# Optimization experiments

Hardware: AMD Instinct MI355X
Metric: run time of the kernel (lower is better)

The kernel has to match this reference:

```python
import jax, jax.numpy as jnp
import numpy as np

TOP_K = 2  # num_expert in the torch module


def setup_inputs() -> dict:
    key = jax.random.key(0)
    ks = jax.random.split(key, 8)
    B, C, H, W, E, Dh = 8, 512, 32, 32, 8, 1024
    inputs = jax.random.normal(ks[0], (B, C, H, W), dtype=jnp.float32)
    k = jax.random.uniform(ks[1], (B, 1, 1, 1), dtype=jnp.float32)
    # gate: global-avg-pool + Linear(C -> E)
    Wg = jax.random.normal(ks[2], (C, E), dtype=jnp.float32) / np.sqrt(C)
    bg = jnp.zeros((E,), dtype=jnp.float32)
    # experts: per-expert 2-layer channel MLP (1x1-conv style), modulated by k
    W1 = jax.random.normal(ks[3], (E, C, Dh), dtype=jnp.float32) / np.sqrt(C)
    b1 = jnp.zeros((E, Dh), dtype=jnp.float32)
    W2 = jax.random.normal(ks[4], (E, Dh, C), dtype=jnp.float32) / np.sqrt(Dh)
    b2 = jnp.zeros((E, C), dtype=jnp.float32)
    return {"inputs": inputs, "k": k, "Wg": Wg, "bg": bg,
            "W1": W1, "b1": b1, "W2": W2, "b2": b2}


def reference(inputs, k, Wg, bg, W1, b1, W2, b2):
    B = inputs.shape[0]
    # --- gate: softmax in fp32, cast back (matches F.softmax(dtype=torch.float)) ---
    logits = jnp.mean(inputs, axis=(2, 3)) @ Wg + bg            # [B, E]
    weights = jax.nn.softmax(logits.astype(jnp.float32), axis=1).astype(inputs.dtype)
    topk_w, topk_idx = jax.lax.top_k(weights, TOP_K)            # [B, K]
    # --- scatter top-k gate weights into dense [B, E] mask (training path) ---
    exp_w = jnp.zeros_like(weights).at[jnp.arange(B)[:, None], topk_idx].set(topk_w)
    # --- run ALL experts densely (training-mode math), masked combine ---
    h = jnp.einsum('bchw,ecd->bedhw', inputs, W1) + b1[None, :, :, None, None]
    h = jax.nn.gelu(h, approximate=False)                        # [B,E,Dh,H,W]
    y = jnp.einsum('bedhw,edc->bechw', h, W2) + b2[None, :, :, None, None]
    y = y * k[:, None]                                           # per-sample scalar mod
    out = inputs + jnp.einsum('bechw,be->bchw', y, exp_w)        # residual + weighted sum
    return out
```

## Files before the change

### kernel.cpp

```cpp
#include <hip/hip_runtime.h>
#include <hip/hip_bf16.h>
#include <math.h>


typedef __bf16 bf16_t;
typedef __attribute__((ext_vector_type(8))) __bf16 bf16x8;
typedef __attribute__((ext_vector_type(4))) __bf16 bf16x4;
typedef __attribute__((ext_vector_type(4))) float f32x4;

#define GLDS(g, l) __builtin_amdgcn_global_load_lds(                      \
    (const __attribute__((address_space(1))) void*)(const void*)(g),       \
    (__attribute__((address_space(3))) void*)(void*)(l), 16, 0, 0)

__device__ __forceinline__ int xcd_swz(int bid, int grid) {
    return (bid & 7) * (grid >> 3) + (bid >> 3);
}

__device__ __forceinline__ float gelu_fast(float x) {
    float z = x * 0.70710678118654752f;
    float az = fabsf(z);
    float t = 1.0f / (1.0f + 0.3275911f * az);
    float p = ((((1.061405429f * t - 1.453152027f) * t + 1.421413741f) * t
                - 0.284496736f) * t + 0.254829592f) * t;
    float e = __expf(-az * az);
    float er = copysignf(1.0f - p * e, z);
    return 0.5f * x * (1.0f + er);
}

__global__ __launch_bounds__(256) void transpose_cvt_all(
    const float* __restrict__ x, const float* __restrict__ W1,
    const float* __restrict__ W2, bf16_t* __restrict__ xT,
    bf16_t* __restrict__ W1t, bf16_t* __restrict__ W2t, float* __restrict__ pp) {
    int id = blockIdx.x;
    const float* src; bf16_t* dst; int Rows, Cols, csh; bool dm = false;
    if (id < 1024)      { src = x;  dst = xT;  Rows = 512;  Cols = 1024; csh = 4; dm = true; }
    else if (id < 2048) { id -= 1024; src = W1; dst = W1t; Rows = 512;  Cols = 1024; csh = 4; }
    else                { id -= 2048; src = W2; dst = W2t; Rows = 1024; Cols = 512; csh = 3; }
    const int bz = id >> 7, t = id & 127;
    const int ct = t & ((1 << csh) - 1), rt = t >> csh;
    const int r0 = rt * 64, c0 = ct * 64;
    __shared__ float tile[64][65];
    const int tid = threadIdx.x;
    const int lrw = tid >> 4, lcol = (tid & 15) * 4;
    const float* sb = src + (size_t)bz * Rows * Cols + c0;
    #pragma unroll
    for (int p = 0; p < 4; ++p) {
        const int row = p * 16 + lrw;
        float4 v = *(const float4*)(sb + (size_t)(r0 + row) * Cols + lcol);
        tile[row][lcol + 0] = v.x; tile[row][lcol + 1] = v.y;
        tile[row][lcol + 2] = v.z; tile[row][lcol + 3] = v.w;
    }
    __syncthreads();
    if (dm) {
        const int row = tid >> 2, q = tid & 3;
        float s = 0.f;
        #pragma unroll
        for (int j = 0; j < 16; ++j) s += tile[row][q * 16 + j];
        s += __shfl_down(s, 2, 4);
        s += __shfl_down(s, 1, 4);
        if (q == 0) pp[(bz * 16 + ct) * 512 + r0 + row] = s;
    }
    bf16_t* db = dst + (size_t)bz * Rows * Cols + r0;
    #pragma unroll
    for (int q = 0; q < 2; ++q) {
        const int idq = q * 256 + tid;
        const int orow = idq >> 3, seg = idq & 7;
        bf16_t ov[8];
        #pragma unroll
        for (int j = 0; j < 8; ++j) ov[j] = (bf16_t)tile[seg * 8 + j][orow];
        *(bf16x8*)(db + (size_t)(c0 + orow) * Rows + seg * 8) = *(bf16x8*)ov;
    }
}

__global__ void gate_kernel(const float* __restrict__ pp, const float* __restrict__ Wg,
                            const float* __restrict__ bg, const float* __restrict__ kmod,
                            int* __restrict__ tidx, float* __restrict__ scale) {
    const int b = blockIdx.x;
    const int tid = threadIdx.x;
    const int lane = tid & 63, wave = tid >> 6;
    float a[8] = {0.f, 0.f, 0.f, 0.f, 0.f, 0.f, 0.f, 0.f};
    #pragma unroll
    for (int rep = 0; rep < 2; ++rep) {
        const int c = rep * 256 + tid;
        float m = 0.f;
        #pragma unroll
        for (int ht = 0; ht < 16; ++ht) m += pp[(b * 16 + ht) * 512 + c];
        #pragma unroll
        for (int e = 0; e < 8; ++e) a[e] += m * Wg[c * 8 + e];
    }
    #pragma unroll
    for (int e = 0; e < 8; ++e)
        #pragma unroll
        for (int off = 32; off; off >>= 1) a[e] += __shfl_xor(a[e], off, 64);
    __shared__ float red[4][8];
    if (lane == 0) {
        #pragma unroll
        for (int e = 0; e < 8; ++e) red[wave][e] = a[e];
    }
    __syncthreads();
    if (tid == 0) {
        float lg[8], mx = -1e30f;
        #pragma unroll
        for (int e = 0; e < 8; ++e) {
            lg[e] = (red[0][e] + red[1][e] + red[2][e] + red[3][e]) * (1.0f / 1024.0f) + bg[e];
            mx = fmaxf(mx, lg[e]);
        }
        float sum = 0.f;
        #pragma unroll
        for (int e = 0; e < 8; ++e) { lg[e] = expf(lg[e] - mx); sum += lg[e]; }
        float inv = 1.0f / sum;
        float best = -1.f; int i0 = 0;
        for (int j = 0; j < 8; ++j) { float w = lg[j] * inv; if (w > best) { best = w; i0 = j; } }
        float best2 = -1.f; int i1 = 0;
        for (int j = 0; j < 8; ++j) { if (j == i0) continue; float w = lg[j] * inv; if (w > best2) { best2 = w; i1 = j; } }
        float kb = kmod[b];
        tidx[b * 2] = i0; tidx[b * 2 + 1] = i1;
        scale[b * 2] = best * kb; scale[b * 2 + 1] = best2 * kb;
    }
}

__global__ __launch_bounds__(256, 4) void gemm1_kernel(
    const bf16_t* __restrict__ W1t, const bf16_t* __restrict__ xT,
    const float* __restrict__ b1, const int* __restrict__ tidx,
    const float* __restrict__ scale, bf16_t* __restrict__ hT) {
    __shared__ bf16_t smem[17408];
    const int bid = xcd_swz(blockIdx.x, 1024);
    const int pair = bid >> 6, rem = bid & 63;
    const int b = pair >> 1, slot = pair & 1;
    const int e = tidx[pair];
    const float s = scale[pair];
    const int d0 = (rem >> 3) * 128, n0 = (rem & 7) * 128;
    const int tid = threadIdx.x;
    const int lane = tid & 63, wave = tid >> 6;
    const int wm = (wave & 1) * 64, wn = (wave >> 1) * 64;
    const int lrow = lane & 15, quad = lane >> 4;

    const bf16_t* gA = W1t + (size_t)e * 524288 + (size_t)d0 * 512;
    const bf16_t* gB = xT + (size_t)b * 524288 + (size_t)n0 * 512;

    f32x4 acc[4][4];
    #pragma unroll
    for (int i = 0; i < 4; ++i)
        #pragma unroll
        for (int j = 0; j < 4; ++j) acc[i][j] = (f32x4){0.f, 0.f, 0.f, 0.f};

    for (int it = 0; it < 8; ++it) {
        const int k0 = it * 64;
        #pragma unroll
        for (int p = 0; p < 4; ++p) {
            const int row = p * 32 + (tid >> 3);
            const int cg = ((tid & 7) ^ (row & 7)) * 8;
            GLDS(gA + (size_t)row * 512 + k0 + cg, smem + (p * 256 + tid) * 8);
            GLDS(gB + (size_t)row * 512 + k0 + cg, smem + 8192 + (p * 256 + tid) * 8);
        }
        __syncthreads();
        #pragma unroll
        for (int kh = 0; kh < 2; ++kh) {
            const int swz = ((kh * 4 + quad) ^ (lrow & 7)) * 8;
            bf16x8 af[4], bfr[4];
            #pragma unroll
            for (int i = 0; i < 4; ++i) {
                af[i]  = *(const bf16x8*)&smem[(wm + i * 16 + lrow) * 64 + swz];
                bfr[i] = *(const bf16x8*)&smem[8192 + (wn + i * 16 + lrow) * 64 + swz];
            }
            #pragma unroll
            for (int i = 0; i < 4; ++i)
                #pragma unroll
                for (int j = 0; j < 4; ++j)
                    acc[i][j] = __builtin_amdgcn_mfma_f32_16x16x32_bf16(af[i], bfr[j], acc[i][j], 0, 0, 0);
        }
        __syncthreads();
    }

    bf16_t* hTb = hT + (size_t)b * 2097152 + slot * 1024;
    #pragma unroll
    for (int i = 0; i < 4; ++i) {
        const int d_l = wm + i * 16 + quad * 4;
        const float4 bb = *(const float4*)(b1 + e * 1024 + d0 + d_l);
        #pragma unroll
        for (int j = 0; j < 4; ++j) {
            const int hw_l = wn + j * 16 + lrow;
            f32x4 a = acc[i][j];
            bf16x4 o = { (bf16_t)(gelu_fast(a[0] + bb.x) * s),
                         (bf16_t)(gelu_fast(a[1] + bb.y) * s),
                         (bf16_t)(gelu_fast(a[2] + bb.z) * s),
                         (bf16_t)(gelu_fast(a[3] + bb.w) * s) };
            *(bf16x4*)&smem[hw_l * 136 + d_l] = o;
        }
    }
    __syncthreads();
    #pragma unroll
    for (int q = 0; q < 8; ++q) {
        const int idx = q * 256 + tid;
        const int row = idx >> 4, c16 = idx & 15;
        bf16x8 v = *(const bf16x8*)&smem[row * 136 + c16 * 8];
        *(bf16x8*)(hTb + (size_t)(n0 + row) * 2048 + d0 + c16 * 8) = v;
    }
}

__global__ __launch_bounds__(256, 2) void gemm2_kernel(
    const bf16_t* __restrict__ W2t, const bf16_t* __restrict__ hT,
    const float* __restrict__ b2, const int* __restrict__ tidx,
    const float* __restrict__ scale, const float* __restrict__ x,
    float* __restrict__ out) {
    __shared__ bf16_t smem[24576];
    const int bid = xcd_swz(blockIdx.x, 512);
    const int b = bid >> 6, rem = bid & 63;
    const int c0 = (rem >> 3) * 64, hw0 = (rem & 7) * 128;
    const int e0 = tidx[b * 2], e1 = tidx[b * 2 + 1];
    const float s0 = scale[b * 2], s1 = scale[b * 2 + 1];
    const int tid = threadIdx.x;
    const int lane = tid & 63, wave = tid >> 6;
    const int wm = (wave & 1) * 64;
    const int wc = (wave >> 1) * 32;
    const int lrow = lane & 15, quad = lane >> 4;

    const bf16_t* hTb = hT + (size_t)b * 2097152 + (size_t)hw0 * 2048;
    const bf16_t* B0 = W2t + (size_t)e0 * 524288 + (size_t)c0 * 1024;
    const bf16_t* B1 = W2t + (size_t)e1 * 524288 + (size_t)c0 * 1024;

    f32x4 acc[4][2];
    #pragma unroll
    for (int i = 0; i < 4; ++i)
        #pragma unroll
        for (int j = 0; j < 2; ++j) acc[i][j] = (f32x4){0.f, 0.f, 0.f, 0.f};

    auto stage = [&](int st, int it) {
        const int k0 = it * 64;
        bf16_t* dst = smem + st * 12288;
        #pragma unroll
        for (int p = 0; p < 4; ++p) {
            const int row = p * 32 + (tid >> 3);
            const int cg = ((tid & 7) ^ (row & 7)) * 8;
            GLDS(hTb + (size_t)row * 2048 + k0 + cg, dst + (p * 256 + tid) * 8);
        }
        const bf16_t* gB = ((it < 16) ? B0 : B1) + (k0 & 1023);
        #pragma unroll
        for (int p = 0; p < 2; ++p) {
            const int row = p * 32 + (tid >> 3);
            const int cg = ((tid & 7) ^ (row & 7)) * 8;
            GLDS(gB + (size_t)row * 1024 + cg, dst + 8192 + (p * 256 + tid) * 8);
        }
    };

    stage(0, 0);
    __syncthreads();

    for (int it = 0; it < 32; ++it) {
        const int cur = it & 1;
        if (it < 31) stage(cur ^ 1, it + 1);
        const bf16_t* cA = smem + cur * 12288;
        const bf16_t* cB = cA + 8192;
        #pragma unroll
        for (int kh = 0; kh < 2; ++kh) {
            const int swz = ((kh * 4 + quad) ^ (lrow & 7)) * 8;
            bf16x8 af[4], bfr[2];
            #pragma unroll
            for (int i = 0; i < 4; ++i)
                af[i] = *(const bf16x8*)&cA[(wm + i * 16 + lrow) * 64 + swz];
            #pragma unroll
            for (int j = 0; j < 2; ++j)
                bfr[j] = *(const bf16x8*)&cB[(wc + j * 16 + lrow) * 64 + swz];
            #pragma unroll
            for (int i = 0; i < 4; ++i)
                #pragma unroll
                for (int j = 0; j < 2; ++j)
                    acc[i][j] = __builtin_amdgcn_mfma_f32_16x16x32_bf16(af[i], bfr[j], acc[i][j], 0, 0, 0);
        }
        __syncthreads();
    }

    #pragma unroll
    for (int j = 0; j < 2; ++j) {
        const int c = c0 + wc + j * 16 + lrow;
        const float bias = s0 * b2[e0 * 512 + c] + s1 * b2[e1 * 512 + c];
        #pragma unroll
        for (int i = 0; i < 4; ++i) {
            const int hw = hw0 + wm + i * 16 + quad * 4;
            const size_t o = ((size_t)(b * 512 + c)) * 1024 + hw;
            const float4 xv = *(const float4*)(x + o);
            float4 ov = { acc[i][j][0] + xv.x + bias, acc[i][j][1] + xv.y + bias,
                          acc[i][j][2] + xv.z + bias, acc[i][j][3] + xv.w + bias };
            *(float4*)(out + o) = ov;
        }
    }
}

extern "C" void kernel_launch(void* const* d_in, const int* in_sizes, int n_in,
                              void* d_out, int out_size, void* d_ws, size_t ws_size,
                              hipStream_t stream) {
    const float* x    = (const float*)d_in[0];
    const float* kmod = (const float*)d_in[1];
    const float* Wg   = (const float*)d_in[2];
    const float* bg   = (const float*)d_in[3];
    const float* W1   = (const float*)d_in[4];
    const float* b1   = (const float*)d_in[5];
    const float* W2   = (const float*)d_in[6];
    const float* b2   = (const float*)d_in[7];
    float* out = (float*)d_out;

    char* ws = (char*)d_ws;
    int*   tix  = (int*)ws;
    float* scl  = (float*)(ws + 64);
    bf16_t* xT  = (bf16_t*)(ws + 32768);
    bf16_t* W1t = (bf16_t*)(ws + 32768 + (size_t)8388608);
    bf16_t* W2t = (bf16_t*)(ws + 32768 + (size_t)2 * 8388608);
    bf16_t* hT  = (bf16_t*)(ws + 32768 + (size_t)3 * 8388608);
    float* pp   = (float*)hT;

    transpose_cvt_all<<<3072, 256, 0, stream>>>(x, W1, W2, xT, W1t, W2t, pp);
    gate_kernel<<<8, 256, 0, stream>>>(pp, Wg, bg, kmod, tix, scl);
    gemm1_kernel<<<1024, 256, 0, stream>>>(W1t, xT, b1, tix, scl, hT);
    gemm2_kernel<<<512, 256, 0, stream>>>(W2t, hT, b2, tix, scl, x, out);
}
```

Baseline: 170.7 us.

## Enlarge gemm1 tiles to 256x256 with double-buffered async LDS loads

```diff
diff --git a/kernel.cpp b/kernel.cpp
--- a/kernel.cpp
+++ b/kernel.cpp
@@ -119,81 +119,114 @@
     }
 }
 
-__global__ __launch_bounds__(256, 4) void gemm1_kernel(
+__global__ __launch_bounds__(512, 2) void gemm1_kernel(
     const bf16_t* __restrict__ W1t, const bf16_t* __restrict__ xT,
     const float* __restrict__ b1, const int* __restrict__ tidx,
     const float* __restrict__ scale, bf16_t* __restrict__ hT) {
-    __shared__ bf16_t smem[17408];
-    const int bid = xcd_swz(blockIdx.x, 1024);
-    const int pair = bid >> 6, rem = bid & 63;
+    __shared__ bf16_t smem[65536];
+    const int bid = xcd_swz(blockIdx.x, 256);
+    const int pair = bid >> 4, rem = bid & 15;
     const int b = pair >> 1, slot = pair & 1;
     const int e = tidx[pair];
     const float s = scale[pair];
-    const int d0 = (rem >> 3) * 128, n0 = (rem & 7) * 128;
+    const int d0 = (rem >> 2) * 256, n0 = (rem & 3) * 256;
     const int tid = threadIdx.x;
     const int lane = tid & 63, wave = tid >> 6;
-    const int wm = (wave & 1) * 64, wn = (wave >> 1) * 64;
+    const int wrr = (wave >> 2) * 128;
+    const int wcc = (wave & 3) * 64;
     const int lrow = lane & 15, quad = lane >> 4;
 
     const bf16_t* gA = W1t + (size_t)e * 524288 + (size_t)d0 * 512;
     const bf16_t* gB = xT + (size_t)b * 524288 + (size_t)n0 * 512;
 
-    f32x4 acc[4][4];
-    #pragma unroll
-    for (int i = 0; i < 4; ++i)
+    f32x4 acc[8][4];
+    #pragma unroll
+    for (int i = 0; i < 8; ++i)
         #pragma unroll
         for (int j = 0; j < 4; ++j) acc[i][j] = (f32x4){0.f, 0.f, 0.f, 0.f};
 
-    for (int it = 0; it < 8; ++it) {
-        const int k0 = it * 64;
-        #pragma unroll
-        for (int p = 0; p < 4; ++p) {
-            const int row = p * 32 + (tid >> 3);
-            const int cg = ((tid & 7) ^ (row & 7)) * 8;
-            GLDS(gA + (size_t)row * 512 + k0 + cg, smem + (p * 256 + tid) * 8);
-            GLDS(gB + (size_t)row * 512 + k0 + cg, smem + 8192 + (p * 256 + tid) * 8);
-        }
-        __syncthreads();
-        #pragma unroll
-        for (int kh = 0; kh < 2; ++kh) {
-            const int swz = ((kh * 4 + quad) ^ (lrow & 7)) * 8;
-            bf16x8 af[4], bfr[4];
-            #pragma unroll
-            for (int i = 0; i < 4; ++i) {
-                af[i]  = *(const bf16x8*)&smem[(wm + i * 16 + lrow) * 64 + swz];
-                bfr[i] = *(const bf16x8*)&smem[8192 + (wn + i * 16 + lrow) * 64 + swz];
-            }
-            #pragma unroll
-            for (int i = 0; i < 4; ++i)
+    auto stage = [&](int st, int kt) {
+        const int k0 = kt * 64;
+        bf16_t* As = smem + st * 16384;
+        bf16_t* Bs = smem + 32768 + st * 16384;
+        #pragma unroll
+        for (int q = 0; q < 4; ++q) {
+            const int idx = q * 512 + tid;
+            const int row = idx >> 3;
+            const int cg = ((idx & 7) ^ (row & 7)) * 8;
+            GLDS(gA + (size_t)row * 512 + k0 + cg, As + idx * 8);
+            GLDS(gB + (size_t)row * 512 + k0 + cg, Bs + idx * 8);
+        }
+    };
+
+    auto compute = [&](int st) {
+        const bf16_t* As = smem + st * 16384;
+        const bf16_t* Bs = smem + 32768 + st * 16384;
+        bf16x8 af[8][2], bf[4][2];
+        #pragma unroll
+        for (int m = 0; m < 8; ++m)
+            #pragma unroll
+            for (int kh = 0; kh < 2; ++kh)
+                af[m][kh] = *(const bf16x8*)&As[(wrr + m * 16 + lrow) * 64
+                                                + (((kh * 4 + quad) ^ (lrow & 7)) * 8)];
+        #pragma unroll
+        for (int n = 0; n < 4; ++n)
+            #pragma unroll
+            for (int kh = 0; kh < 2; ++kh)
+                bf[n][kh] = *(const bf16x8*)&Bs[(wcc + n * 16 + lrow) * 64
+                                                + (((kh * 4 + quad) ^ (lrow & 7)) * 8)];
+        #pragma unroll
+        for (int m = 0; m < 8; ++m)
+            #pragma unroll
+            for (int n = 0; n < 4; ++n)
                 #pragma unroll
-                for (int j = 0; j < 4; ++j)
-                    acc[i][j] = __builtin_amdgcn_mfma_f32_16x16x32_bf16(af[i], bfr[j], acc[i][j], 0, 0, 0);
-        }
-        __syncthreads();
-    }
-
-    bf16_t* hTb = hT + (size_t)b * 2097152 + slot * 1024;
-    #pragma unroll
-    for (int i = 0; i < 4; ++i) {
-        const int d_l = wm + i * 16 + quad * 4;
+                for (int kh = 0; kh < 2; ++kh)
+                    acc[m][n] = __builtin_amdgcn_mfma_f32_16x16x32_bf16(
+                        af[m][kh], bf[n][kh], acc[m][n], 0, 0, 0);
+    };
+
+    stage(0, 0);
+    stage(1, 1);
+    asm volatile("s_waitcnt vmcnt(8)" ::: "memory");
+    __builtin_amdgcn_s_barrier();
+
+    #pragma unroll
+    for (int kt = 0; kt < 8; ++kt) {
+        const int cur = kt & 1;
+        compute(cur);
+        __builtin_amdgcn_s_barrier();
+        if (kt < 6) {
+            stage(cur, kt + 2);
+            asm volatile("s_waitcnt vmcnt(8)" ::: "memory");
+        } else if (kt == 6) {
+            asm volatile("s_waitcnt vmcnt(0)" ::: "memory");
+        }
+        __builtin_amdgcn_s_barrier();
+    }
+
+    bf16_t* eb = smem;
+    #pragma unroll
+    for (int m = 0; m < 8; ++m) {
+        const int d_l = wrr + m * 16 + quad * 4;
         const float4 bb = *(const float4*)(b1 + e * 1024 + d0 + d_l);
         #pragma unroll
-        for (int j = 0; j < 4; ++j) {
-            const int hw_l = wn + j * 16 + lrow;
-            f32x4 a = acc[i][j];
+        for (int n = 0; n < 4; ++n) {
+            const int hw_l = wcc + n * 16 + lrow;
+            f32x4 a = acc[m][n];
             bf16x4 o = { (bf16_t)(gelu_fast(a[0] + bb.x) * s),
                          (bf16_t)(gelu_fast(a[1] + bb.y) * s),
                          (bf16_t)(gelu_fast(a[2] + bb.z) * s),
                          (bf16_t)(gelu_fast(a[3] + bb.w) * s) };
-            *(bf16x4*)&smem[hw_l * 136 + d_l] = o;
+            *(bf16x4*)&eb[hw_l * 256 + (d_l ^ ((hw_l & 7) << 3))] = o;
         }
     }
     __syncthreads();
-    #pragma unroll
-    for (int q = 0; q < 8; ++q) {
-        const int idx = q * 256 + tid;
-        const int row = idx >> 4, c16 = idx & 15;
-        bf16x8 v = *(const bf16x8*)&smem[row * 136 + c16 * 8];
+    bf16_t* hTb = hT + (size_t)b * 2097152 + slot * 1024;
+    #pragma unroll
+    for (int q = 0; q < 16; ++q) {
+        const int idx = q * 512 + tid;
+        const int row = idx >> 5, c16 = idx & 31;
+        bf16x8 v = *(const bf16x8*)&eb[row * 256 + ((c16 * 8) ^ ((row & 7) << 3))];
         *(bf16x8*)(hTb + (size_t)(n0 + row) * 2048 + d0 + c16 * 8) = v;
     }
 }
@@ -310,6 +343,6 @@
 
     transpose_cvt_all<<<3072, 256, 0, stream>>>(x, W1, W2, xT, W1t, W2t, pp);
     gate_kernel<<<8, 256, 0, stream>>>(pp, Wg, bg, kmod, tix, scl);
-    gemm1_kernel<<<1024, 256, 0, stream>>>(W1t, xT, b1, tix, scl, hT);
+    gemm1_kernel<<<256, 512, 0, stream>>>(W1t, xT, b1, tix, scl, hT);
     gemm2_kernel<<<512, 256, 0, stream>>>(W2t, hT, b2, tix, scl, x, out);
 }
```

After: 189.6 us. 11.1% more time.
